# Performance work log

Hardware: AMD Instinct MI355X
Metric: run time of the kernel (lower is better)

The kernel has to match this reference:

```python
import jax, jax.numpy as jnp
import numpy as np

EMBED_DIM = 2048
HEAD_DIM = 128
B, T = 4, 2048


def setup_inputs() -> dict:
    key = jax.random.key(0)
    k1, k2, k3, k4 = jax.random.split(key, 4)
    x_in = jax.random.normal(k1, (B, T, EMBED_DIM), dtype=jnp.float32)
    scale = 1.0 / np.sqrt(EMBED_DIM)
    Wq = jax.random.normal(k2, (EMBED_DIM, HEAD_DIM), dtype=jnp.float32) * scale
    Wk = jax.random.normal(k3, (EMBED_DIM, HEAD_DIM), dtype=jnp.float32) * scale
    Wv = jax.random.normal(k4, (EMBED_DIM, HEAD_DIM), dtype=jnp.float32) * scale
    return {"x_in": x_in, "Wq": Wq, "Wk": Wk, "Wv": Wv}


def reference(x_in, Wq, Wk, Wv):
    # x_in: [B, T, E]; projections (Linear, no bias)
    q = jnp.einsum('bte,ed->btd', x_in, Wq)  # [B,T,D]
    k = jnp.einsum('bte,ed->btd', x_in, Wk)
    v = jnp.einsum('bte,ed->btd', x_in, Wv)
    t = x_in.shape[1]
    d = Wq.shape[1]
    s = jnp.einsum('btd,bsd->bts', q, k) / jnp.sqrt(jnp.asarray(d, q.dtype))  # [B,Tq,Tk]
    # causal mask: positions with tril==0 (k index > q index) -> -inf
    causal = jnp.tril(jnp.ones((t, t), dtype=bool))
    s = jnp.where(causal, s, -jnp.inf)
    # NOTE: original module applies softmax over dim=1 (query axis), faithfully reproduced
    a = jax.nn.softmax(s, axis=1)
    z = jnp.einsum('bts,bsd->btd', a, v)  # [B,T,D]
    return z
```

## Files before the change

kernel.cpp:

```cpp
#include <hip/hip_runtime.h>

typedef _Float16 f16x8 __attribute__((ext_vector_type(8)));
typedef _Float16 f16x4 __attribute__((ext_vector_type(4)));
typedef float f32x4 __attribute__((ext_vector_type(4)));

#define T_DIM 2048
#define E_DIM 2048
#define D_DIM 128
#define NB 4
#define KSP_P 4
#define KCH_P 512
#define KSP_A 8
#define KCH_A 256

__device__ __forceinline__ void gll16(const void* g, void* l) {
  __builtin_amdgcn_global_load_lds(
      (const __attribute__((address_space(1))) unsigned int*)g,
      (__attribute__((address_space(3))) unsigned int*)l, 16, 0, 0);
}


__global__ void prep(const float* __restrict__ Wq, const float* __restrict__ Wk,
                     const float* __restrict__ Wv, _Float16* __restrict__ WhT,
                     float* __restrict__ Z, float* __restrict__ L) {
  int idx = blockIdx.x * 256 + threadIdx.x;
  int y = blockIdx.y;
  if (y < 3) {
    const float* W = (y == 0) ? Wq : ((y == 1) ? Wk : Wv);
    int e = idx & (E_DIM - 1), d = idx >> 11;
    WhT[(size_t)y * (D_DIM * E_DIM) + idx] = (_Float16)W[e * D_DIM + d];
  } else {
    f32x4 z = {0.f, 0.f, 0.f, 0.f};
    *(f32x4*)(Z + (size_t)idx * 4) = z;
    if (idx < NB * T_DIM) L[idx] = 0.f;
  }
}


__global__ __launch_bounds__(768) void proj_gemm(
    const float* __restrict__ x, const _Float16* __restrict__ WhT,
    _Float16* __restrict__ Ph) {
  __shared__ _Float16 A16[2][128 * 64];
  __shared__ _Float16 Bsw[2][384 * 64];
  const int tid = threadIdx.x, w = tid >> 6, lane = tid & 63;
  const int wn = w >> 1, wr = w & 1, quad = lane >> 4, l16 = lane & 15;
  const int t0 = blockIdx.x * 128;
  const int ks = blockIdx.y;
  const int kb = ks * KCH_P;
  const int arow = tid >> 2, ac16 = (tid & 3) * 16;
  const int as0 = ((tid & 3) * 2) ^ (arow & 7);
  const int as1 = ((tid & 3) * 2 + 1) ^ (arow & 7);

  f32x4 ax0, ax1, ax2, ax3;
  auto loadA = [&](int k0) {
    if (tid < 512) {
      const float* src = x + (size_t)(t0 + arow) * E_DIM + k0 + ac16;
      ax0 = *(const f32x4*)src;
      ax1 = *(const f32x4*)(src + 4);
      ax2 = *(const f32x4*)(src + 8);
      ax3 = *(const f32x4*)(src + 12);
    }
  };
  auto writeA = [&](int buf) {
    if (tid < 512) {
      f16x8 o0, o1;
#pragma unroll
      for (int e = 0; e < 4; ++e) {
        o0[e] = (_Float16)ax0[e];
        o0[e + 4] = (_Float16)ax1[e];
        o1[e] = (_Float16)ax2[e];
        o1[e + 4] = (_Float16)ax3[e];
      }
      *(f16x8*)(&A16[buf][arow * 64 + as0 * 8]) = o0;
      *(f16x8*)(&A16[buf][arow * 64 + as1 * 8]) = o1;
    }
  };
  auto stageB = [&](int buf, int k0) {
#pragma unroll
    for (int p = 0; p < 4; ++p) {
      int item = p * 768 + tid;
      int row = item >> 3, seg = item & 7;
      int g = seg ^ (row & 7);
      gll16(WhT + (size_t)row * E_DIM + k0 + g * 8, &Bsw[buf][item * 8]);
    }
  };

  f32x4 acc[4][4] = {};
  loadA(kb);
  stageB(0, kb);
  asm volatile("s_waitcnt vmcnt(0)" ::: "memory");
  writeA(0);
  const int NIT = KCH_P / 64;
  for (int it = 0; it < NIT; ++it) {
    const int cur = it & 1;
    __syncthreads();
    if (it + 1 < NIT) {
      loadA(kb + (it + 1) * 64);
      stageB(cur ^ 1, kb + (it + 1) * 64);
    }
    __builtin_amdgcn_s_setprio(1);
#pragma unroll
    for (int kq = 0; kq < 2; ++kq) {
      f16x8 af[4], bf[4];
#pragma unroll
      for (int i = 0; i < 4; ++i) {
        int row = wr * 64 + i * 16 + l16;
        int sg = ((kq * 4 + quad) ^ (row & 7)) * 8;
        af[i] = *(const f16x8*)(&A16[cur][row * 64 + sg]);
      }
#pragma unroll
      for (int j = 0; j < 4; ++j) {
        int row = wn * 64 + j * 16 + l16;
        int sg = ((kq * 4 + quad) ^ (row & 7)) * 8;
        bf[j] = *(const f16x8*)(&Bsw[cur][row * 64 + sg]);
      }
#pragma unroll
      for (int i = 0; i < 4; ++i)
#pragma unroll
        for (int j = 0; j < 4; ++j)
          acc[i][j] = __builtin_amdgcn_mfma_f32_16x16x32_f16(af[i], bf[j], acc[i][j], 0, 0, 0);
    }
    __builtin_amdgcn_s_setprio(0);
    if (it + 1 < NIT) {
      asm volatile("s_waitcnt vmcnt(0)" ::: "memory");
      writeA(cur ^ 1);
    }
  }
  const int mat = wn >> 1;
  const int nb0 = (wn & 1) * 64;
  _Float16* P = Ph + ((size_t)(ks * 3 + mat) << 20);
  if (mat < 2) {
#pragma unroll
    for (int i = 0; i < 4; ++i)
#pragma unroll
      for (int j = 0; j < 4; ++j) {
        int n = nb0 + j * 16 + l16;
#pragma unroll
        for (int r = 0; r < 4; ++r) {
          int t = t0 + wr * 64 + i * 16 + quad * 4 + r;
          P[(size_t)t * D_DIM + n] = (_Float16)acc[i][j][r];
        }
      }
  } else {
#pragma unroll
    for (int i = 0; i < 4; ++i)
#pragma unroll
      for (int j = 0; j < 4; ++j) {
        int n = nb0 + j * 16 + l16;
        int t = t0 + wr * 64 + i * 16 + quad * 4;
        f16x4 o;
#pragma unroll
        for (int r = 0; r < 4; ++r) o[r] = (_Float16)acc[i][j][r];
        *(f16x4*)(P + ((size_t)(t >> 11) * D_DIM + n) * T_DIM + (t & (T_DIM - 1))) = o;
      }
  }
}


__global__ void proj_reduce(const _Float16* __restrict__ Ph, _Float16* __restrict__ Qh,
                            _Float16* __restrict__ Kh, _Float16* __restrict__ VT) {
  size_t u = ((size_t)blockIdx.x * 256 + threadIdx.x) * 8;
  int mat = (int)(u >> 20);
  size_t rem = u & ((1u << 20) - 1);
  float s[8] = {};
#pragma unroll
  for (int ks = 0; ks < KSP_P; ++ks) {
    f16x8 p = *(const f16x8*)(Ph + ((size_t)(ks * 3 + mat) << 20) + rem);
#pragma unroll
    for (int e = 0; e < 8; ++e) s[e] += (float)p[e];
  }
  f16x8 o;
#pragma unroll
  for (int e = 0; e < 8; ++e) o[e] = (_Float16)s[e];
  _Float16* dst = (mat == 0) ? Qh : ((mat == 1) ? Kh : VT);
  *(f16x8*)(dst + rem) = o;
}


__global__ __launch_bounds__(256) void s_gemm(const _Float16* __restrict__ Qh,
                                              const _Float16* __restrict__ Kh,
                                              _Float16* __restrict__ S,
                                              float* __restrict__ L) {
  int idx = blockIdx.x;
  int xt = (int)((sqrtf(8.f * idx + 1.f) - 1.f) * 0.5f);
  while ((xt + 1) * (xt + 2) / 2 <= idx) ++xt;
  while (xt * (xt + 1) / 2 > idx) --xt;
  int yt = idx - xt * (xt + 1) / 2;
  __shared__ _Float16 As_[4][128 * 32];
  __shared__ _Float16 Bs[4][128 * 32];
  const int tid = threadIdx.x, w = tid >> 6, lane = tid & 63;
  const int wr = w >> 1, wc = w & 1, quad = lane >> 4, l16 = lane & 15;
  const int t0 = xt * 128, s0 = yt * 128, b = blockIdx.y;
  const _Float16* A = Qh + (size_t)b * T_DIM * D_DIM;
  const _Float16* B = Kh + (size_t)b * T_DIM * D_DIM;
  const int srow = lane >> 2;
  const int swz = ((lane & 3) ^ ((srow >> 1) & 3)) * 8;
#pragma unroll
  for (int kq = 0; kq < 4; ++kq)
#pragma unroll
    for (int q = 0; q < 2; ++q) {
      int rbase = w * 32 + q * 16;
      gll16(A + (size_t)(t0 + rbase + srow) * D_DIM + kq * 32 + swz,
            As_[kq] + rbase * 32);
      gll16(B + (size_t)(s0 + rbase + srow) * D_DIM + kq * 32 + swz,
            Bs[kq] + rbase * 32);
    }
  __syncthreads();
  f32x4 acc[4][4] = {};
  const int bsg = (quad ^ ((l16 >> 1) & 3)) * 8;
#pragma unroll
  for (int kq = 0; kq < 4; ++kq) {
    f16x8 af[4], bf[4];
#pragma unroll
    for (int i = 0; i < 4; ++i)
      af[i] = *(const f16x8*)(As_[kq] + (wr * 64 + i * 16 + l16) * 32 + bsg);
#pragma unroll
    for (int j = 0; j < 4; ++j)
      bf[j] = *(const f16x8*)(Bs[kq] + (wc * 64 + j * 16 + l16) * 32 + bsg);
#pragma unroll
    for (int i = 0; i < 4; ++i)
#pragma unroll
      for (int j = 0; j < 4; ++j)
        acc[i][j] = __builtin_amdgcn_mfma_f32_16x16x32_f16(af[i], bf[j], acc[i][j], 0, 0, 0);
  }
  _Float16* Sb = S + (size_t)b * T_DIM * T_DIM;
  const float scale = 0.08838834764831845f;
#pragma unroll
  for (int j = 0; j < 4; ++j) {
    const int s = s0 + wc * 64 + j * 16 + l16;
    float l = 0.f;
#pragma unroll
    for (int i = 0; i < 4; ++i)
#pragma unroll
      for (int r = 0; r < 4; ++r) {
        int t = t0 + wr * 64 + i * 16 + quad * 4 + r;
        float e = (s > t) ? 0.f : __expf(acc[i][j][r] * scale);
        Sb[(size_t)t * T_DIM + s] = (_Float16)e;
        l += e;
      }
    l += __shfl_xor(l, 16, 64);
    l += __shfl_xor(l, 32, 64);
    if (quad == 0) atomicAdd(&L[(size_t)b * T_DIM + s], l);
  }
}


__global__ __launch_bounds__(256) void av_gemm(const _Float16* __restrict__ S,
                                               const _Float16* __restrict__ VT,
                                               const float* __restrict__ L,
                                               float* __restrict__ Z) {
  const int t0 = blockIdx.x * 128, b = blockIdx.y, ks = blockIdx.z;
  const int Kmax = t0 + 128;
  const int Kstart = ks * KCH_A;
  if (Kstart >= Kmax) return;
  const int Kend = (Kstart + KCH_A < Kmax) ? (Kstart + KCH_A) : Kmax;
  const int nit = (Kend - Kstart) >> 5;
  __shared__ _Float16 As[2][128 * 32];
  __shared__ _Float16 Bs[2][128 * 32];
  __shared__ float Ls[KCH_A];
  const int tid = threadIdx.x, w = tid >> 6, lane = tid & 63;
  const int wr = w >> 1, wc = w & 1, quad = lane >> 4, l16 = lane & 15;
  const _Float16* Sb = S + (size_t)b * T_DIM * T_DIM;
  const _Float16* Vb = VT + (size_t)b * D_DIM * T_DIM;
  for (int i = tid; i < Kend - Kstart; i += 256)
    Ls[i] = 1.f / L[b * T_DIM + Kstart + i];
  const int srow = lane >> 2;
  const int arow = tid >> 2, aseg = tid & 3;
  const int asw = (aseg ^ ((arow >> 1) & 3)) * 8;
  f16x8 sv0, sv1;
  auto loadS = [&](int k0) {
    sv0 = *(const f16x8*)(Sb + (size_t)(t0 + arow) * T_DIM + k0 + aseg * 8);
    sv1 = *(const f16x8*)(Sb + (size_t)(t0 + 64 + arow) * T_DIM + k0 + aseg * 8);
  };
  auto stageB = [&](int buf, int k0) {
#pragma unroll
    for (int q = 0; q < 2; ++q) {
      int rbase = w * 32 + q * 16;
      int row = rbase + srow;
      int g = ((lane & 3) ^ ((row >> 1) & 3)) * 8;
      gll16(Vb + (size_t)row * T_DIM + k0 + g, Bs[buf] + rbase * 32);
    }
  };
  auto writeA = [&](int buf, int k0) {
#pragma unroll
    for (int q = 0; q < 2; ++q) {
      f16x8 v = q ? sv1 : sv0;
      f16x8 o;
#pragma unroll
      for (int e = 0; e < 8; ++e) {
        int li = k0 + aseg * 8 + e - Kstart;
        o[e] = (_Float16)((float)v[e] * Ls[li]);
      }
      *(f16x8*)(As[buf] + (q * 64 + arow) * 32 + asw) = o;
    }
  };
  f32x4 acc[4][4] = {};
  __syncthreads();
  loadS(Kstart);
  stageB(0, Kstart);
  asm volatile("s_waitcnt vmcnt(0)" ::: "memory");
  writeA(0, Kstart);
  for (int it = 0; it < nit; ++it) {
    const int cur = it & 1;
    const int k0 = Kstart + it * 32;
    __syncthreads();
    if (it + 1 < nit) {
      loadS(k0 + 32);
      stageB(cur ^ 1, k0 + 32);
    }
    f16x8 af[4], bf[4];
#pragma unroll
    for (int i = 0; i < 4; ++i) {
      int row = wr * 64 + i * 16 + l16;
      int sg = (quad ^ ((row >> 1) & 3)) * 8;
      af[i] = *(const f16x8*)(As[cur] + row * 32 + sg);
    }
#pragma unroll
    for (int j = 0; j < 4; ++j) {
      int row = wc * 64 + j * 16 + l16;
      int sg = (quad ^ ((row >> 1) & 3)) * 8;
      bf[j] = *(const f16x8*)(Bs[cur] + row * 32 + sg);
    }
    __builtin_amdgcn_s_setprio(1);
#pragma unroll
    for (int i = 0; i < 4; ++i)
#pragma unroll
      for (int j = 0; j < 4; ++j)
        acc[i][j] = __builtin_amdgcn_mfma_f32_16x16x32_f16(af[i], bf[j], acc[i][j], 0, 0, 0);
    __builtin_amdgcn_s_setprio(0);
    if (it + 1 < nit) {
      asm volatile("s_waitcnt vmcnt(0)" ::: "memory");
      writeA(cur ^ 1, k0 + 32);
    }
  }
  float* Zb = Z + (size_t)b * T_DIM * D_DIM;
#pragma unroll
  for (int i = 0; i < 4; ++i)
#pragma unroll
    for (int j = 0; j < 4; ++j) {
      int n = wc * 64 + j * 16 + l16;
#pragma unroll
      for (int r = 0; r < 4; ++r) {
        int t = t0 + wr * 64 + i * 16 + quad * 4 + r;
        atomicAdd(&Zb[(size_t)t * D_DIM + n], acc[i][j][r]);
      }
    }
}


extern "C" void kernel_launch(void* const* d_in, const int* in_sizes, int n_in,
                              void* d_out, int out_size, void* d_ws, size_t ws_size,
                              hipStream_t stream) {
  const float* x = (const float*)d_in[0];
  const float* Wq = (const float*)d_in[1];
  const float* Wk = (const float*)d_in[2];
  const float* Wv = (const float*)d_in[3];
  char* ws = (char*)d_ws;
  _Float16* Ph = (_Float16*)(ws);
  _Float16* S = (_Float16*)(ws);
  _Float16* WhT = (_Float16*)(ws + 33554432);
  _Float16* Qh = (_Float16*)(ws + 35127296);
  _Float16* Kh = (_Float16*)(ws + 37224448);
  _Float16* VT = (_Float16*)(ws + 39321600);
  float* L = (float*)(ws + 41418752);
  float* Z = (float*)d_out;

  prep<<<dim3(1024, 4), 256, 0, stream>>>(Wq, Wk, Wv, WhT, Z, L);
  proj_gemm<<<dim3(64, KSP_P), 768, 0, stream>>>(x, WhT, Ph);
  proj_reduce<<<1536, 256, 0, stream>>>(Ph, Qh, Kh, VT);
  s_gemm<<<dim3(136, 4), 256, 0, stream>>>(Qh, Kh, S, L);
  av_gemm<<<dim3(16, 4, KSP_A), 256, 0, stream>>>(S, VT, L, Z);
}
```

Measured before the change: 158.4 us.

## Fold softmax column normalization into V and stream S directly to LDS

The 1/L column normalization moves from the S operand onto V, since dividing column s of S is the same as scaling row s of V. A new scale_v kernel writes a scaled copy of V. With the A operand no longer needing per-element rescaling, av_gemm loads both S and V straight into LDS asynchronously and uses a K tile of 64 with an XOR swizzle, removing the register round trip and the per-element multiply in the main loop. This costs an extra kernel launch, an extra pass over V, and twice the LDS per block, which may reduce occupancy.

```diff
diff --git a/kernel.cpp b/kernel.cpp
--- a/kernel.cpp
+++ b/kernel.cpp
@@ -245,93 +245,80 @@
 }
 
 
+__global__ void scale_v(const _Float16* __restrict__ VT, const float* __restrict__ L,
+                        _Float16* __restrict__ VTs) {
+  int idx = blockIdx.x * 256 + threadIdx.x;
+  int b = idx >> 15;
+  int rem = idx & 32767;
+  int s8 = (rem & 255) * 8;
+  int d = rem >> 8;
+  size_t base = ((size_t)b * D_DIM + d) * T_DIM + s8;
+  f16x8 v = *(const f16x8*)(VT + base);
+  const float* Lp = L + (size_t)b * T_DIM + s8;
+  f16x8 o;
+#pragma unroll
+  for (int e = 0; e < 8; ++e) o[e] = (_Float16)((float)v[e] / Lp[e]);
+  *(f16x8*)(VTs + base) = o;
+}
+
+
 __global__ __launch_bounds__(256) void av_gemm(const _Float16* __restrict__ S,
-                                               const _Float16* __restrict__ VT,
-                                               const float* __restrict__ L,
+                                               const _Float16* __restrict__ VTs,
                                                float* __restrict__ Z) {
   const int t0 = blockIdx.x * 128, b = blockIdx.y, ks = blockIdx.z;
   const int Kmax = t0 + 128;
   const int Kstart = ks * KCH_A;
   if (Kstart >= Kmax) return;
   const int Kend = (Kstart + KCH_A < Kmax) ? (Kstart + KCH_A) : Kmax;
-  const int nit = (Kend - Kstart) >> 5;
-  __shared__ _Float16 As[2][128 * 32];
-  __shared__ _Float16 Bs[2][128 * 32];
-  __shared__ float Ls[KCH_A];
+  const int nit = (Kend - Kstart) >> 6;
+  __shared__ _Float16 As[2][128 * 64];
+  __shared__ _Float16 Bs[2][128 * 64];
   const int tid = threadIdx.x, w = tid >> 6, lane = tid & 63;
   const int wr = w >> 1, wc = w & 1, quad = lane >> 4, l16 = lane & 15;
   const _Float16* Sb = S + (size_t)b * T_DIM * T_DIM;
-  const _Float16* Vb = VT + (size_t)b * D_DIM * T_DIM;
-  for (int i = tid; i < Kend - Kstart; i += 256)
-    Ls[i] = 1.f / L[b * T_DIM + Kstart + i];
-  const int srow = lane >> 2;
-  const int arow = tid >> 2, aseg = tid & 3;
-  const int asw = (aseg ^ ((arow >> 1) & 3)) * 8;
-  f16x8 sv0, sv1;
-  auto loadS = [&](int k0) {
-    sv0 = *(const f16x8*)(Sb + (size_t)(t0 + arow) * T_DIM + k0 + aseg * 8);
-    sv1 = *(const f16x8*)(Sb + (size_t)(t0 + 64 + arow) * T_DIM + k0 + aseg * 8);
+  const _Float16* Vb = VTs + (size_t)b * D_DIM * T_DIM;
+
+  auto stage = [&](int buf, int k0) {
+#pragma unroll
+    for (int p = 0; p < 4; ++p) {
+      int item = p * 256 + tid;
+      int row = item >> 3, seg = item & 7;
+      int g = (seg ^ (row & 7)) * 8;
+      gll16(Sb + (size_t)(t0 + row) * T_DIM + k0 + g, &As[buf][item * 8]);
+      gll16(Vb + (size_t)row * T_DIM + k0 + g, &Bs[buf][item * 8]);
+    }
   };
-  auto stageB = [&](int buf, int k0) {
-#pragma unroll
-    for (int q = 0; q < 2; ++q) {
-      int rbase = w * 32 + q * 16;
-      int row = rbase + srow;
-      int g = ((lane & 3) ^ ((row >> 1) & 3)) * 8;
-      gll16(Vb + (size_t)row * T_DIM + k0 + g, Bs[buf] + rbase * 32);
-    }
-  };
-  auto writeA = [&](int buf, int k0) {
-#pragma unroll
-    for (int q = 0; q < 2; ++q) {
-      f16x8 v = q ? sv1 : sv0;
-      f16x8 o;
-#pragma unroll
-      for (int e = 0; e < 8; ++e) {
-        int li = k0 + aseg * 8 + e - Kstart;
-        o[e] = (_Float16)((float)v[e] * Ls[li]);
-      }
-      *(f16x8*)(As[buf] + (q * 64 + arow) * 32 + asw) = o;
-    }
-  };
+
   f32x4 acc[4][4] = {};
-  __syncthreads();
-  loadS(Kstart);
-  stageB(0, Kstart);
-  asm volatile("s_waitcnt vmcnt(0)" ::: "memory");
-  writeA(0, Kstart);
+  stage(0, Kstart);
   for (int it = 0; it < nit; ++it) {
     const int cur = it & 1;
-    const int k0 = Kstart + it * 32;
+    asm volatile("s_waitcnt vmcnt(0)" ::: "memory");
     __syncthreads();
-    if (it + 1 < nit) {
-      loadS(k0 + 32);
-      stageB(cur ^ 1, k0 + 32);
-    }
-    f16x8 af[4], bf[4];
-#pragma unroll
-    for (int i = 0; i < 4; ++i) {
-      int row = wr * 64 + i * 16 + l16;
-      int sg = (quad ^ ((row >> 1) & 3)) * 8;
-      af[i] = *(const f16x8*)(As[cur] + row * 32 + sg);
-    }
-#pragma unroll
-    for (int j = 0; j < 4; ++j) {
-      int row = wc * 64 + j * 16 + l16;
-      int sg = (quad ^ ((row >> 1) & 3)) * 8;
-      bf[j] = *(const f16x8*)(Bs[cur] + row * 32 + sg);
-    }
+    if (it + 1 < nit) stage(cur ^ 1, Kstart + (it + 1) * 64);
     __builtin_amdgcn_s_setprio(1);
 #pragma unroll
-    for (int i = 0; i < 4; ++i)
-#pragma unroll
-      for (int j = 0; j < 4; ++j)
-        acc[i][j] = __builtin_amdgcn_mfma_f32_16x16x32_f16(af[i], bf[j], acc[i][j], 0, 0, 0);
+    for (int kq = 0; kq < 2; ++kq) {
+      f16x8 af[4], bf[4];
+#pragma unroll
+      for (int i = 0; i < 4; ++i) {
+        int row = wr * 64 + i * 16 + l16;
+        int sg = ((kq * 4 + quad) ^ (row & 7)) * 8;
+        af[i] = *(const f16x8*)(&As[cur][row * 64 + sg]);
+      }
+#pragma unroll
+      for (int j = 0; j < 4; ++j) {
+        int row = wc * 64 + j * 16 + l16;
+        int sg = ((kq * 4 + quad) ^ (row & 7)) * 8;
+        bf[j] = *(const f16x8*)(&Bs[cur][row * 64 + sg]);
+      }
+#pragma unroll
+      for (int i = 0; i < 4; ++i)
+#pragma unroll
+        for (int j = 0; j < 4; ++j)
+          acc[i][j] = __builtin_amdgcn_mfma_f32_16x16x32_f16(af[i], bf[j], acc[i][j], 0, 0, 0);
+    }
     __builtin_amdgcn_s_setprio(0);
-    if (it + 1 < nit) {
-      asm volatile("s_waitcnt vmcnt(0)" ::: "memory");
-      writeA(cur ^ 1, k0 + 32);
-    }
   }
   float* Zb = Z + (size_t)b * T_DIM * D_DIM;
 #pragma unroll
@@ -363,11 +350,13 @@
   _Float16* Kh = (_Float16*)(ws + 37224448);
   _Float16* VT = (_Float16*)(ws + 39321600);
   float* L = (float*)(ws + 41418752);
+  _Float16* VTs = (_Float16*)(ws + 41451520);
   float* Z = (float*)d_out;
 
   prep<<<dim3(1024, 4), 256, 0, stream>>>(Wq, Wk, Wv, WhT, Z, L);
   proj_gemm<<<dim3(64, KSP_P), 768, 0, stream>>>(x, WhT, Ph);
   proj_reduce<<<1536, 256, 0, stream>>>(Ph, Qh, Kh, VT);
   s_gemm<<<dim3(136, 4), 256, 0, stream>>>(Qh, Kh, S, L);
-  av_gemm<<<dim3(16, 4, KSP_A), 256, 0, stream>>>(S, VT, L, Z);
-}
+  scale_v<<<512, 256, 0, stream>>>(VT, L, VTs);
+  av_gemm<<<dim3(16, 4, KSP_A), 256, 0, stream>>>(S, VTs, Z);
+}
```

New measurement: 161.4 us. About the same (+1.9%).

## Launch av_gemm over lower-triangular 128x128 tiles only with fixed K chunk

Applied to the files above, without the earlier changes.

The AV GEMM grid changes from 16x4x8 blocks with K-split chunks of 256, where many blocks exit early, to 136 triangular tile blocks per batch. Each block covers a single 128-wide K chunk. A row/column tile index is decoded from the linear block id with a sqrt-based inverse. This removes idle early-exit blocks and evens out per-block work, but doubles the number of partial-sum atomic accumulations into Z.

```diff
diff --git a/kernel.cpp b/kernel.cpp
--- a/kernel.cpp
+++ b/kernel.cpp
@@ -10,8 +10,6 @@
 #define NB 4
 #define KSP_P 4
 #define KCH_P 512
-#define KSP_A 8
-#define KCH_A 256
 
 __device__ __forceinline__ void gll16(const void* g, void* l) {
   __builtin_amdgcn_global_load_lds(
@@ -249,21 +247,21 @@
                                                const _Float16* __restrict__ VT,
                                                const float* __restrict__ L,
                                                float* __restrict__ Z) {
-  const int t0 = blockIdx.x * 128, b = blockIdx.y, ks = blockIdx.z;
-  const int Kmax = t0 + 128;
-  const int Kstart = ks * KCH_A;
-  if (Kstart >= Kmax) return;
-  const int Kend = (Kstart + KCH_A < Kmax) ? (Kstart + KCH_A) : Kmax;
-  const int nit = (Kend - Kstart) >> 5;
+  int idx = blockIdx.x;
+  int xt = (int)((sqrtf(8.f * idx + 1.f) - 1.f) * 0.5f);
+  while ((xt + 1) * (xt + 2) / 2 <= idx) ++xt;
+  while (xt * (xt + 1) / 2 > idx) --xt;
+  int yt = idx - xt * (xt + 1) / 2;
+  const int t0 = xt * 128, b = blockIdx.y;
+  const int kbase = yt * 128;
   __shared__ _Float16 As[2][128 * 32];
   __shared__ _Float16 Bs[2][128 * 32];
-  __shared__ float Ls[KCH_A];
+  __shared__ float Ls[128];
   const int tid = threadIdx.x, w = tid >> 6, lane = tid & 63;
   const int wr = w >> 1, wc = w & 1, quad = lane >> 4, l16 = lane & 15;
   const _Float16* Sb = S + (size_t)b * T_DIM * T_DIM;
   const _Float16* Vb = VT + (size_t)b * D_DIM * T_DIM;
-  for (int i = tid; i < Kend - Kstart; i += 256)
-    Ls[i] = 1.f / L[b * T_DIM + Kstart + i];
+  if (tid < 128) Ls[tid] = 1.f / L[(size_t)b * T_DIM + kbase + tid];
   const int srow = lane >> 2;
   const int arow = tid >> 2, aseg = tid & 3;
   const int asw = (aseg ^ ((arow >> 1) & 3)) * 8;
@@ -288,7 +286,7 @@
       f16x8 o;
 #pragma unroll
       for (int e = 0; e < 8; ++e) {
-        int li = k0 + aseg * 8 + e - Kstart;
+        int li = (k0 - kbase) + aseg * 8 + e;
         o[e] = (_Float16)((float)v[e] * Ls[li]);
       }
       *(f16x8*)(As[buf] + (q * 64 + arow) * 32 + asw) = o;
@@ -296,13 +294,14 @@
   };
   f32x4 acc[4][4] = {};
   __syncthreads();
-  loadS(Kstart);
-  stageB(0, Kstart);
+  loadS(kbase);
+  stageB(0, kbase);
   asm volatile("s_waitcnt vmcnt(0)" ::: "memory");
-  writeA(0, Kstart);
+  writeA(0, kbase);
+  const int nit = 4;
   for (int it = 0; it < nit; ++it) {
     const int cur = it & 1;
-    const int k0 = Kstart + it * 32;
+    const int k0 = kbase + it * 32;
     __syncthreads();
     if (it + 1 < nit) {
       loadS(k0 + 32);
@@ -369,5 +368,5 @@
   proj_gemm<<<dim3(64, KSP_P), 768, 0, stream>>>(x, WhT, Ph);
   proj_reduce<<<1536, 256, 0, stream>>>(Ph, Qh, Kh, VT);
   s_gemm<<<dim3(136, 4), 256, 0, stream>>>(Qh, Kh, S, L);
-  av_gemm<<<dim3(16, 4, KSP_A), 256, 0, stream>>>(S, VT, L, Z);
-}
+  av_gemm<<<dim3(136, 4), 256, 0, stream>>>(S, VT, L, Z);
+}
```

New measurement: 178.0 us. +12.4%, slower.
